# Optimization experiments

Hardware: AMD Instinct MI355X
Metric: run time of the kernel (lower is better)

The kernel has to match this reference:

```python
import jax, jax.numpy as jnp
import numpy as np
import math

HIDDEN = 1024
NUM_HEADS = 16
HEAD_DIM = HIDDEN // NUM_HEADS


def _rope_tables(seq_len, dim, dtype):
    inv_freq = 1.0 / (10000.0 ** (np.arange(0, dim, 2, dtype=np.float32) / dim))
    t = np.arange(seq_len, dtype=np.float32)
    freqs = np.einsum('i,j->ij', t, inv_freq)          # [S, dim/2]
    emb = np.concatenate([freqs, freqs], axis=-1)      # [S, dim]
    return jnp.asarray(np.cos(emb), dtype), jnp.asarray(np.sin(emb), dtype)


def _rotate_half(x):
    x1, x2 = x[..., : x.shape[-1] // 2], x[..., x.shape[-1] // 2:]
    return jnp.concatenate([-x2, x1], axis=-1)


def setup_inputs() -> dict:
    key = jax.random.key(0)
    k1, k2, k3 = jax.random.split(key, 3)
    B, S = 2, 2048
    x = jax.random.normal(k1, (B, S, HIDDEN), dtype=jnp.float32)
    attention_mask = jnp.ones((B, S), dtype=jnp.int32)
    w_qkv = jax.random.normal(k2, (HIDDEN, 3 * HIDDEN), dtype=jnp.float32) * (1.0 / math.sqrt(HIDDEN))
    w_out = jax.random.normal(k3, (HIDDEN, HIDDEN), dtype=jnp.float32) * (1.0 / math.sqrt(HIDDEN))
    return {"x": x, "attention_mask": attention_mask, "w_qkv": w_qkv, "w_out": w_out}


def reference(x, attention_mask, w_qkv, w_out):
    B, S, H = x.shape
    qkv = x @ w_qkv                                   # [B,S,3H]
    qkv = qkv.reshape(B, S, NUM_HEADS, 3 * HEAD_DIM).transpose(0, 2, 1, 3)  # [B,h,S,3d]
    q, k, v = jnp.split(qkv, 3, axis=-1)              # each [B,h,S,d]
    cos, sin = _rope_tables(S, HEAD_DIM, x.dtype)     # [S,d]
    cos = cos[None, None]
    sin = sin[None, None]
    q = q * cos + _rotate_half(q) * sin
    k = k * cos + _rotate_half(k) * sin
    scale = math.sqrt(HEAD_DIM)
    scores = jnp.einsum('bhqd,bhkd->bhqk', q, k) / scale  # [B,h,S,S]
    mask_value = jnp.finfo(scores.dtype).min
    scores = jnp.where(attention_mask[:, None, None, :] == 0, mask_value, scores)
    attn = jax.nn.softmax(scores, axis=-1)
    context = jnp.einsum('bhqk,bhkd->bhqd', attn, v)  # [B,h,S,d]
    context = context.transpose(0, 2, 1, 3).reshape(B, S, H)
    return context @ w_out
```

## Files before the change

### kernel.cpp

```cpp
#include <hip/hip_runtime.h>
#include <hip/hip_bf16.h>
#include <math.h>
#include <stdint.h>


typedef __bf16 bf16;
typedef __bf16 bf16x8 __attribute__((ext_vector_type(8)));
typedef __bf16 bf16x4 __attribute__((ext_vector_type(4)));
typedef float f32x4 __attribute__((ext_vector_type(4)));

#define AS1 __attribute__((address_space(1)))
#define AS3 __attribute__((address_space(3)))

__device__ __forceinline__ void gload_lds16(const void* g, void* l) {
  __builtin_amdgcn_global_load_lds((const AS1 void*)g, (AS3 void*)l, 16, 0, 0);
}

__device__ __forceinline__ f32x4 mfma16(bf16x8 a, bf16x8 b, f32x4 c) {
  return __builtin_amdgcn_mfma_f32_16x16x32_bf16(a, b, c, 0, 0, 0);
}

#define S_LEN 2048


__global__ void k_split_x(const float* __restrict__ x, bf16* __restrict__ xh,
                          bf16* __restrict__ xl) {
  int i = blockIdx.x * 256 + threadIdx.x;
  float4 v = ((const float4*)x)[i];
  float vv[4] = {v.x, v.y, v.z, v.w};
  bf16x4 h, l;
#pragma unroll
  for (int j = 0; j < 4; j++) {
    bf16 hb = (bf16)vv[j];
    h[j] = hb;
    l[j] = (bf16)(vv[j] - (float)hb);
  }
  ((bf16x4*)xh)[i] = h;
  ((bf16x4*)xl)[i] = l;
}

__global__ void k_wt_qkv(const float* __restrict__ w, bf16* __restrict__ bth,
                         bf16* __restrict__ btl) {
  __shared__ float t[32][33];
  int n0 = blockIdx.x * 32, k0 = blockIdx.y * 32;
  int tx = threadIdx.x & 31, ty = threadIdx.x >> 5;
#pragma unroll
  for (int i = 0; i < 4; i++)
    t[ty + 8 * i][tx] = w[(size_t)(k0 + ty + 8 * i) * 3072 + n0 + tx];
  __syncthreads();
#pragma unroll
  for (int i = 0; i < 4; i++) {
    int r = ty + 8 * i;
    float v = t[tx][r];
    size_t o = (size_t)(n0 + r) * 1024 + k0 + tx;
    bf16 hb = (bf16)v;
    bth[o] = hb;
    btl[o] = (bf16)(v - (float)hb);
  }
}

__global__ void k_wt_out(const float* __restrict__ w, bf16* __restrict__ bt) {
  __shared__ float t[32][33];
  int n0 = blockIdx.x * 32, k0 = blockIdx.y * 32;
  int tx = threadIdx.x & 31, ty = threadIdx.x >> 5;
#pragma unroll
  for (int i = 0; i < 4; i++)
    t[ty + 8 * i][tx] = w[(size_t)(k0 + ty + 8 * i) * 1024 + n0 + tx];
  __syncthreads();
#pragma unroll
  for (int i = 0; i < 4; i++) {
    int r = ty + 8 * i;
    bt[(size_t)(n0 + r) * 1024 + k0 + tx] = (bf16)t[tx][r];
  }
}

__global__ void k_rope_tables(float* __restrict__ ct, float* __restrict__ st) {
  int i = blockIdx.x * 256 + threadIdx.x;
  int s = i >> 5, j = i & 31;
  double invf = pow(10000.0, -(double)j / 32.0);
  double a = (double)s * invf;
  ct[i] = (float)cos(a);
  st[i] = (float)sin(a);
}

__global__ __launch_bounds__(256, 2) void k_gemm_qkv(
    const bf16* __restrict__ Ah, const bf16* __restrict__ Al,
    const bf16* __restrict__ Bh, const bf16* __restrict__ Bl,
    bf16* __restrict__ C) {
  const int K = 1024, N = 3072;
  __shared__ __align__(16) bf16 sAh[128 * 32];
  __shared__ __align__(16) bf16 sAl[128 * 32];
  __shared__ __align__(16) bf16 sBh[128 * 32];
  __shared__ __align__(16) bf16 sBl[128 * 32];
  int tid = threadIdx.x, lane = tid & 63, wid = tid >> 6;
  int m0 = blockIdx.x * 128, n0 = blockIdx.y * 128;
  int wm = wid >> 1, wn = wid & 1;

  f32x4 acc[4][4];
#pragma unroll
  for (int a = 0; a < 4; a++)
#pragma unroll
    for (int b = 0; b < 4; b++) acc[a][b] = (f32x4){0.f, 0.f, 0.f, 0.f};

  for (int k0 = 0; k0 < K; k0 += 32) {
#pragma unroll
    for (int p = 0; p < 2; p++) {
      int slot = p * 256 + tid;
      int row = slot >> 2, c16 = slot & 3;
      int cs = c16 ^ ((row >> 1) & 3);
      char* lb = (char*)nullptr;
      int ldsoff = (p * 256 + wid * 64) * 16;
      size_t ga = (size_t)(m0 + row) * K + k0 + cs * 8;
      size_t gb = (size_t)(n0 + row) * K + k0 + cs * 8;
      (void)lb;
      gload_lds16(Ah + ga, (char*)sAh + ldsoff);
      gload_lds16(Al + ga, (char*)sAl + ldsoff);
      gload_lds16(Bh + gb, (char*)sBh + ldsoff);
      gload_lds16(Bl + gb, (char*)sBl + ldsoff);
    }
    __syncthreads();

    bf16x8 fah[4], fal[4], fbh[4], fbl[4];
#pragma unroll
    for (int mf = 0; mf < 4; mf++) {
      int row = wm * 64 + mf * 16 + (lane & 15);
      int c16 = (lane >> 4) ^ ((row >> 1) & 3);
      int off = row * 64 + c16 * 16;
      fah[mf] = *(const bf16x8*)((const char*)sAh + off);
      fal[mf] = *(const bf16x8*)((const char*)sAl + off);
    }
#pragma unroll
    for (int nf = 0; nf < 4; nf++) {
      int row = wn * 64 + nf * 16 + (lane & 15);
      int c16 = (lane >> 4) ^ ((row >> 1) & 3);
      int off = row * 64 + c16 * 16;
      fbh[nf] = *(const bf16x8*)((const char*)sBh + off);
      fbl[nf] = *(const bf16x8*)((const char*)sBl + off);
    }
#pragma unroll
    for (int mf = 0; mf < 4; mf++)
#pragma unroll
      for (int nf = 0; nf < 4; nf++) {
        acc[mf][nf] = mfma16(fah[mf], fbh[nf], acc[mf][nf]);
        acc[mf][nf] = mfma16(fah[mf], fbl[nf], acc[mf][nf]);
        acc[mf][nf] = mfma16(fal[mf], fbh[nf], acc[mf][nf]);
      }
    __syncthreads();
  }

#pragma unroll
  for (int mf = 0; mf < 4; mf++)
#pragma unroll
    for (int nf = 0; nf < 4; nf++)
#pragma unroll
      for (int r = 0; r < 4; r++) {
        int row = m0 + wm * 64 + mf * 16 + (lane >> 4) * 4 + r;
        int col = n0 + wn * 64 + nf * 16 + (lane & 15);
        C[(size_t)row * N + col] = (bf16)acc[mf][nf][r];
      }
}

__global__ void k_rope_scatter(const bf16* __restrict__ QKV,
                               const float* __restrict__ ct,
                               const float* __restrict__ st,
                               bf16* __restrict__ Q, bf16* __restrict__ Kb,
                               bf16* __restrict__ Vt) {
  __shared__ __align__(16) bf16 vt[64 * 64];
  int sblk = blockIdx.x, bh = blockIdx.y;
  int b = bh >> 4, h = bh & 15;
  int tid = threadIdx.x;
  int r = tid >> 2, c = tid & 3;
  int s = sblk * 64 + r;
  size_t rowbase = ((size_t)(b * S_LEN + s)) * 3072 + h * 192;

  bf16x8 qlo = *(const bf16x8*)(QKV + rowbase + c * 8);
  bf16x8 qhi = *(const bf16x8*)(QKV + rowbase + c * 8 + 32);
  bf16x8 klo = *(const bf16x8*)(QKV + rowbase + 64 + c * 8);
  bf16x8 khi = *(const bf16x8*)(QKV + rowbase + 64 + c * 8 + 32);
  bf16x8 vlo = *(const bf16x8*)(QKV + rowbase + 128 + c * 8);
  bf16x8 vhi = *(const bf16x8*)(QKV + rowbase + 128 + c * 8 + 32);

  bf16x8 qol, qoh, kol, koh;
#pragma unroll
  for (int j = 0; j < 8; j++) {
    float cs = ct[s * 32 + c * 8 + j], sn = st[s * 32 + c * 8 + j];
    float q1 = (float)qlo[j], q2 = (float)qhi[j];
    qol[j] = (bf16)(q1 * cs - q2 * sn);
    qoh[j] = (bf16)(q2 * cs + q1 * sn);
    float k1 = (float)klo[j], k2 = (float)khi[j];
    kol[j] = (bf16)(k1 * cs - k2 * sn);
    koh[j] = (bf16)(k2 * cs + k1 * sn);
  }
  size_t qb = ((size_t)bh * S_LEN + s) * 64 + c * 8;
  *(bf16x8*)(Q + qb) = qol;
  *(bf16x8*)(Q + qb + 32) = qoh;
  *(bf16x8*)(Kb + qb) = kol;
  *(bf16x8*)(Kb + qb + 32) = koh;

#pragma unroll
  for (int j = 0; j < 8; j++) {
    vt[(c * 8 + j) * 64 + r] = vlo[j];
    vt[(c * 8 + 32 + j) * 64 + r] = vhi[j];
  }
  __syncthreads();
  int d = tid >> 2, cc = tid & 3;
  size_t vb = ((size_t)bh * 64 + d) * S_LEN + sblk * 64 + cc * 16;
  *(bf16x8*)(Vt + vb) = *(const bf16x8*)(vt + d * 64 + cc * 16);
  *(bf16x8*)(Vt + vb + 8) = *(const bf16x8*)(vt + d * 64 + cc * 16 + 8);
}

__global__ __launch_bounds__(256, 2) void k_attn(
    const bf16* __restrict__ Q, const bf16* __restrict__ Kb,
    const bf16* __restrict__ Vt, const int* __restrict__ mask,
    bf16* __restrict__ Ctx) {
  __shared__ __align__(16) bf16 sK[128 * 64];
  __shared__ __align__(16) bf16 sV[64 * 128];
  __shared__ __align__(16) bf16 sP[4 * 32 * 128];
  int tid = threadIdx.x, lane = tid & 63, wid = tid >> 6;
  int qt = blockIdx.x, bh = blockIdx.y;
  int b = bh >> 4, h = bh & 15;
  int q0 = qt * 128;

  bf16x8 aQ[2][2];
#pragma unroll
  for (int mf = 0; mf < 2; mf++)
#pragma unroll
    for (int ks = 0; ks < 2; ks++) {
      const bf16* p = Q + ((size_t)bh * S_LEN + q0 + wid * 32 + mf * 16 + (lane & 15)) * 64 +
                      ks * 32 + (lane >> 4) * 8;
      bf16x8 v = *(const bf16x8*)p;
#pragma unroll
      for (int j = 0; j < 8; j++) v[j] = (bf16)((float)v[j] * 0.125f);
      aQ[mf][ks] = v;
    }

  f32x4 O[2][4];
  float mrow[2][4], lrow[2][4];
#pragma unroll
  for (int mf = 0; mf < 2; mf++)
#pragma unroll
    for (int nd = 0; nd < 4; nd++) O[mf][nd] = (f32x4){0.f, 0.f, 0.f, 0.f};
#pragma unroll
  for (int mf = 0; mf < 2; mf++)
#pragma unroll
    for (int r = 0; r < 4; r++) { mrow[mf][r] = -3e38f; lrow[mf][r] = 0.f; }

  for (int kt = 0; kt < 16; kt++) {
    int k0 = kt * 128;
#pragma unroll
    for (int p = 0; p < 4; p++) {
      int slot = p * 256 + tid;
      int row = slot >> 3, c16 = slot & 7;
      int cs = c16 ^ (row & 7);
      gload_lds16(Kb + ((size_t)bh * S_LEN + k0 + row) * 64 + cs * 8,
                  (char*)sK + (p * 256 + wid * 64) * 16);
    }
#pragma unroll
    for (int p = 0; p < 4; p++) {
      int slot = p * 256 + tid;
      int row = slot >> 4, c16 = slot & 15;
      int cs = c16 ^ (row & 7);
      gload_lds16(Vt + ((size_t)bh * 64 + row) * S_LEN + k0 + cs * 8,
                  (char*)sV + (p * 256 + wid * 64) * 16);
    }
    __syncthreads();

    f32x4 sfr[2][8];
#pragma unroll
    for (int mf = 0; mf < 2; mf++)
#pragma unroll
      for (int nf = 0; nf < 8; nf++) sfr[mf][nf] = (f32x4){0.f, 0.f, 0.f, 0.f};
#pragma unroll
    for (int nf = 0; nf < 8; nf++) {
#pragma unroll
      for (int ks = 0; ks < 2; ks++) {
        int row = nf * 16 + (lane & 15);
        int c16 = (ks * 4 + (lane >> 4)) ^ (row & 7);
        bf16x8 bk = *(const bf16x8*)((const char*)sK + row * 128 + c16 * 16);
        sfr[0][nf] = mfma16(aQ[0][ks], bk, sfr[0][nf]);
        sfr[1][nf] = mfma16(aQ[1][ks], bk, sfr[1][nf]);
      }
    }
#pragma unroll
    for (int nf = 0; nf < 8; nf++) {
      int kpos = k0 + nf * 16 + (lane & 15);
      if (mask[b * S_LEN + kpos] == 0) {
#pragma unroll
        for (int r = 0; r < 4; r++) { sfr[0][nf][r] = -1e30f; sfr[1][nf][r] = -1e30f; }
      }
    }
    float alpha[2][4];
#pragma unroll
    for (int mf = 0; mf < 2; mf++)
#pragma unroll
      for (int r = 0; r < 4; r++) {
        float mx = -3e38f;
#pragma unroll
        for (int nf = 0; nf < 8; nf++) mx = fmaxf(mx, sfr[mf][nf][r]);
#pragma unroll
        for (int off = 1; off < 16; off <<= 1) mx = fmaxf(mx, __shfl_xor(mx, off, 64));
        float mnew = fmaxf(mrow[mf][r], mx);
        float a = __expf(mrow[mf][r] - mnew);
        mrow[mf][r] = mnew;
        float psum = 0.f;
#pragma unroll
        for (int nf = 0; nf < 8; nf++) {
          float p0 = __expf(sfr[mf][nf][r] - mnew);
          sfr[mf][nf][r] = p0;
          psum += p0;
        }
#pragma unroll
        for (int off = 1; off < 16; off <<= 1) psum += __shfl_xor(psum, off, 64);
        lrow[mf][r] = lrow[mf][r] * a + psum;
        alpha[mf][r] = a;
      }
#pragma unroll
    for (int mf = 0; mf < 2; mf++)
#pragma unroll
      for (int nd = 0; nd < 4; nd++)
#pragma unroll
        for (int r = 0; r < 4; r++) O[mf][nd][r] *= alpha[mf][r];

    char* pw = (char*)sP + wid * 32 * 256;
#pragma unroll
    for (int mf = 0; mf < 2; mf++)
#pragma unroll
      for (int r = 0; r < 4; r++) {
        int row = mf * 16 + (lane >> 4) * 4 + r;
#pragma unroll
        for (int nf = 0; nf < 8; nf++) {
          int col = nf * 16 + (lane & 15);
          int c16 = (col >> 3) ^ (row & 7);
          *(bf16*)(pw + row * 256 + c16 * 16 + (col & 7) * 2) = (bf16)sfr[mf][nf][r];
        }
      }
#pragma unroll
    for (int ks = 0; ks < 4; ks++) {
      bf16x8 aP[2];
#pragma unroll
      for (int mf = 0; mf < 2; mf++) {
        int row = mf * 16 + (lane & 15);
        int c16 = (ks * 4 + (lane >> 4)) ^ (row & 7);
        aP[mf] = *(const bf16x8*)(pw + row * 256 + c16 * 16);
      }
#pragma unroll
      for (int nd = 0; nd < 4; nd++) {
        int row = nd * 16 + (lane & 15);
        int c16 = (ks * 4 + (lane >> 4)) ^ (row & 7);
        bf16x8 bv = *(const bf16x8*)((const char*)sV + row * 256 + c16 * 16);
#pragma unroll
        for (int mf = 0; mf < 2; mf++) O[mf][nd] = mfma16(aP[mf], bv, O[mf][nd]);
      }
    }
    __syncthreads();
  }

#pragma unroll
  for (int mf = 0; mf < 2; mf++)
#pragma unroll
    for (int r = 0; r < 4; r++) {
      float inv = 1.f / lrow[mf][r];
      int srow = q0 + wid * 32 + mf * 16 + (lane >> 4) * 4 + r;
#pragma unroll
      for (int nd = 0; nd < 4; nd++) {
        int d = nd * 16 + (lane & 15);
        Ctx[((size_t)b * S_LEN + srow) * 1024 + h * 64 + d] = (bf16)(O[mf][nd][r] * inv);
      }
    }
}

__global__ __launch_bounds__(256, 2) void k_gemm_out(
    const bf16* __restrict__ A, const bf16* __restrict__ Bt,
    float* __restrict__ C) {
  const int K = 1024, N = 1024;
  __shared__ __align__(16) bf16 sA[128 * 32];
  __shared__ __align__(16) bf16 sB[128 * 32];
  int tid = threadIdx.x, lane = tid & 63, wid = tid >> 6;
  int m0 = blockIdx.x * 128, n0 = blockIdx.y * 128;
  int wm = wid >> 1, wn = wid & 1;

  f32x4 acc[4][4];
#pragma unroll
  for (int a = 0; a < 4; a++)
#pragma unroll
    for (int b = 0; b < 4; b++) acc[a][b] = (f32x4){0.f, 0.f, 0.f, 0.f};

  for (int k0 = 0; k0 < K; k0 += 32) {
#pragma unroll
    for (int p = 0; p < 2; p++) {
      int slot = p * 256 + tid;
      int row = slot >> 2, c16 = slot & 3;
      int cs = c16 ^ ((row >> 1) & 3);
      int ldsoff = (p * 256 + wid * 64) * 16;
      gload_lds16(A + (size_t)(m0 + row) * K + k0 + cs * 8, (char*)sA + ldsoff);
      gload_lds16(Bt + (size_t)(n0 + row) * K + k0 + cs * 8, (char*)sB + ldsoff);
    }
    __syncthreads();
    bf16x8 fa[4], fb[4];
#pragma unroll
    for (int mf = 0; mf < 4; mf++) {
      int row = wm * 64 + mf * 16 + (lane & 15);
      int c16 = (lane >> 4) ^ ((row >> 1) & 3);
      fa[mf] = *(const bf16x8*)((const char*)sA + row * 64 + c16 * 16);
    }
#pragma unroll
    for (int nf = 0; nf < 4; nf++) {
      int row = wn * 64 + nf * 16 + (lane & 15);
      int c16 = (lane >> 4) ^ ((row >> 1) & 3);
      fb[nf] = *(const bf16x8*)((const char*)sB + row * 64 + c16 * 16);
    }
#pragma unroll
    for (int mf = 0; mf < 4; mf++)
#pragma unroll
      for (int nf = 0; nf < 4; nf++)
        acc[mf][nf] = mfma16(fa[mf], fb[nf], acc[mf][nf]);
    __syncthreads();
  }
#pragma unroll
  for (int mf = 0; mf < 4; mf++)
#pragma unroll
    for (int nf = 0; nf < 4; nf++)
#pragma unroll
      for (int r = 0; r < 4; r++) {
        int row = m0 + wm * 64 + mf * 16 + (lane >> 4) * 4 + r;
        int col = n0 + wn * 64 + nf * 16 + (lane & 15);
        C[(size_t)row * N + col] = acc[mf][nf][r];
      }
}

extern "C" void kernel_launch(void* const* d_in, const int* in_sizes, int n_in,
                              void* d_out, int out_size, void* d_ws, size_t ws_size,
                              hipStream_t stream) {
  const float* x = (const float*)d_in[0];
  const int* mask = (const int*)d_in[1];
  const float* wqkv = (const float*)d_in[2];
  const float* wout = (const float*)d_in[3];
  float* out = (float*)d_out;
  char* ws = (char*)d_ws;

  bf16* Xh  = (bf16*)(ws + 0);
  bf16* Xl  = (bf16*)(ws + 8388608);
  bf16* Wqh = (bf16*)(ws + 16777216);
  bf16* Wql = (bf16*)(ws + 23068672);
  bf16* Wo  = (bf16*)(ws + 29360128);
  bf16* QKV = (bf16*)(ws + 31457280);
  bf16* Qb  = (bf16*)(ws + 56623104);
  bf16* Kb  = (bf16*)(ws + 65011712);
  bf16* Vt  = (bf16*)(ws + 73400320);
  bf16* Ctx = (bf16*)(ws + 81788928);
  float* ct = (float*)(ws + 90177536);
  float* st = (float*)(ws + 90439680);

  k_split_x<<<4096, 256, 0, stream>>>(x, Xh, Xl);
  k_wt_qkv<<<dim3(96, 32), 256, 0, stream>>>(wqkv, Wqh, Wql);
  k_wt_out<<<dim3(32, 32), 256, 0, stream>>>(wout, Wo);
  k_rope_tables<<<256, 256, 0, stream>>>(ct, st);
  k_gemm_qkv<<<dim3(32, 24), 256, 0, stream>>>(Xh, Xl, Wqh, Wql, QKV);
  k_rope_scatter<<<dim3(32, 32), 256, 0, stream>>>(QKV, ct, st, Qb, Kb, Vt);
  k_attn<<<dim3(16, 32), 256, 0, stream>>>(Qb, Kb, Vt, mask, Ctx);
  k_gemm_out<<<dim3(32, 8), 256, 0, stream>>>(Ctx, Wo, out);
}
```

Measured before the change: 285.9 us.

## Transpose attention MFMAs to keep P in registers and drop LDS staging

The attention kernel now computes S^T = K·Q^T, so each lane holds scores for a single query row across keys. Softmax reductions need only two cross-lane shuffles instead of four per row, and the probability tile feeds the PV MFMA straight from registers, which removes the sP shared-memory buffer and its scattered bf16 writes. Mask loads become int4 vectors, output stores become bf16x4, and launch bounds ask for 3 blocks per CU now that less LDS is used. In exchange V is read from LDS as two bf16x4 halves per fragment, and the tighter launch bound may force register spills.

```diff
diff --git a/kernel.cpp b/kernel.cpp
--- a/kernel.cpp
+++ b/kernel.cpp
@@ -108,11 +108,9 @@
       int slot = p * 256 + tid;
       int row = slot >> 2, c16 = slot & 3;
       int cs = c16 ^ ((row >> 1) & 3);
-      char* lb = (char*)nullptr;
       int ldsoff = (p * 256 + wid * 64) * 16;
       size_t ga = (size_t)(m0 + row) * K + k0 + cs * 8;
       size_t gb = (size_t)(n0 + row) * K + k0 + cs * 8;
-      (void)lb;
       gload_lds16(Ah + ga, (char*)sAh + ldsoff);
       gload_lds16(Al + ga, (char*)sAl + ldsoff);
       gload_lds16(Bh + gb, (char*)sBh + ldsoff);
@@ -209,41 +207,39 @@
   *(bf16x8*)(Vt + vb + 8) = *(const bf16x8*)(vt + d * 64 + cc * 16 + 8);
 }
 
-__global__ __launch_bounds__(256, 2) void k_attn(
+__global__ __launch_bounds__(256, 3) void k_attn(
     const bf16* __restrict__ Q, const bf16* __restrict__ Kb,
     const bf16* __restrict__ Vt, const int* __restrict__ mask,
     bf16* __restrict__ Ctx) {
   __shared__ __align__(16) bf16 sK[128 * 64];
   __shared__ __align__(16) bf16 sV[64 * 128];
-  __shared__ __align__(16) bf16 sP[4 * 32 * 128];
   int tid = threadIdx.x, lane = tid & 63, wid = tid >> 6;
+  int g = lane >> 4, q = lane & 15;
   int qt = blockIdx.x, bh = blockIdx.y;
   int b = bh >> 4, h = bh & 15;
-  int q0 = qt * 128;
-
-  bf16x8 aQ[2][2];
+  int q0 = qt * 128 + wid * 32;
+
+  bf16x8 bQ[2][2];
 #pragma unroll
   for (int mf = 0; mf < 2; mf++)
 #pragma unroll
     for (int ks = 0; ks < 2; ks++) {
-      const bf16* p = Q + ((size_t)bh * S_LEN + q0 + wid * 32 + mf * 16 + (lane & 15)) * 64 +
-                      ks * 32 + (lane >> 4) * 8;
+      const bf16* p = Q + ((size_t)bh * S_LEN + q0 + mf * 16 + q) * 64 + ks * 32 + g * 8;
       bf16x8 v = *(const bf16x8*)p;
 #pragma unroll
       for (int j = 0; j < 8; j++) v[j] = (bf16)((float)v[j] * 0.125f);
-      aQ[mf][ks] = v;
+      bQ[mf][ks] = v;
     }
 
   f32x4 O[2][4];
-  float mrow[2][4], lrow[2][4];
-#pragma unroll
-  for (int mf = 0; mf < 2; mf++)
+  float mrow[2], lrow[2];
+#pragma unroll
+  for (int mf = 0; mf < 2; mf++) {
 #pragma unroll
     for (int nd = 0; nd < 4; nd++) O[mf][nd] = (f32x4){0.f, 0.f, 0.f, 0.f};
-#pragma unroll
-  for (int mf = 0; mf < 2; mf++)
-#pragma unroll
-    for (int r = 0; r < 4; r++) { mrow[mf][r] = -3e38f; lrow[mf][r] = 0.f; }
+    mrow[mf] = -3e38f;
+    lrow[mf] = 0.f;
+  }
 
   for (int kt = 0; kt < 16; kt++) {
     int k0 = kt * 128;
@@ -269,104 +265,96 @@
 #pragma unroll
     for (int mf = 0; mf < 2; mf++)
 #pragma unroll
-      for (int nf = 0; nf < 8; nf++) sfr[mf][nf] = (f32x4){0.f, 0.f, 0.f, 0.f};
-#pragma unroll
-    for (int nf = 0; nf < 8; nf++) {
+      for (int kf = 0; kf < 8; kf++) sfr[mf][kf] = (f32x4){0.f, 0.f, 0.f, 0.f};
+#pragma unroll
+    for (int kf = 0; kf < 8; kf++) {
 #pragma unroll
       for (int ks = 0; ks < 2; ks++) {
-        int row = nf * 16 + (lane & 15);
-        int c16 = (ks * 4 + (lane >> 4)) ^ (row & 7);
-        bf16x8 bk = *(const bf16x8*)((const char*)sK + row * 128 + c16 * 16);
-        sfr[0][nf] = mfma16(aQ[0][ks], bk, sfr[0][nf]);
-        sfr[1][nf] = mfma16(aQ[1][ks], bk, sfr[1][nf]);
+        int row = kf * 16 + q;
+        int c16 = (ks * 4 + g) ^ (row & 7);
+        bf16x8 ak = *(const bf16x8*)((const char*)sK + row * 128 + c16 * 16);
+        sfr[0][kf] = mfma16(ak, bQ[0][ks], sfr[0][kf]);
+        sfr[1][kf] = mfma16(ak, bQ[1][ks], sfr[1][kf]);
       }
     }
 #pragma unroll
-    for (int nf = 0; nf < 8; nf++) {
-      int kpos = k0 + nf * 16 + (lane & 15);
-      if (mask[b * S_LEN + kpos] == 0) {
-#pragma unroll
-        for (int r = 0; r < 4; r++) { sfr[0][nf][r] = -1e30f; sfr[1][nf][r] = -1e30f; }
+    for (int kf = 0; kf < 8; kf++) {
+      int4 mv = *(const int4*)(mask + b * S_LEN + k0 + kf * 16 + g * 4);
+      int mm[4] = {mv.x, mv.y, mv.z, mv.w};
+#pragma unroll
+      for (int r = 0; r < 4; r++)
+        if (mm[r] == 0) { sfr[0][kf][r] = -1e30f; sfr[1][kf][r] = -1e30f; }
+    }
+    float alpha[2];
+#pragma unroll
+    for (int mf = 0; mf < 2; mf++) {
+      float mx = -3e38f;
+#pragma unroll
+      for (int kf = 0; kf < 8; kf++)
+#pragma unroll
+        for (int r = 0; r < 4; r++) mx = fmaxf(mx, sfr[mf][kf][r]);
+      mx = fmaxf(mx, __shfl_xor(mx, 16, 64));
+      mx = fmaxf(mx, __shfl_xor(mx, 32, 64));
+      float mnew = fmaxf(mrow[mf], mx);
+      float al = __expf(mrow[mf] - mnew);
+      mrow[mf] = mnew;
+      float ps = 0.f;
+#pragma unroll
+      for (int kf = 0; kf < 8; kf++)
+#pragma unroll
+        for (int r = 0; r < 4; r++) {
+          float p0 = __expf(sfr[mf][kf][r] - mnew);
+          sfr[mf][kf][r] = p0;
+          ps += p0;
+        }
+      ps += __shfl_xor(ps, 16, 64);
+      ps += __shfl_xor(ps, 32, 64);
+      lrow[mf] = lrow[mf] * al + ps;
+      alpha[mf] = al;
+    }
+#pragma unroll
+    for (int mf = 0; mf < 2; mf++)
+#pragma unroll
+      for (int nd = 0; nd < 4; nd++)
+#pragma unroll
+        for (int r = 0; r < 4; r++) O[mf][nd][r] *= alpha[mf];
+
+#pragma unroll
+    for (int ks = 0; ks < 4; ks++) {
+      bf16x8 pb[2];
+#pragma unroll
+      for (int mf = 0; mf < 2; mf++)
+#pragma unroll
+        for (int j = 0; j < 8; j++)
+          pb[mf][j] = (bf16)sfr[mf][2 * ks + (j >> 2)][j & 3];
+#pragma unroll
+      for (int nd = 0; nd < 4; nd++) {
+        int row = nd * 16 + q;
+        int sw = (row & 7) << 4;
+        bf16x4 v0 = *(const bf16x4*)((const char*)sV + row * 256 + ((ks * 64 + g * 8) ^ sw));
+        bf16x4 v1 = *(const bf16x4*)((const char*)sV + row * 256 + ((ks * 64 + g * 8 + 32) ^ sw));
+        bf16x8 av;
+#pragma unroll
+        for (int j = 0; j < 4; j++) { av[j] = v0[j]; av[4 + j] = v1[j]; }
+#pragma unroll
+        for (int mf = 0; mf < 2; mf++) O[mf][nd] = mfma16(av, pb[mf], O[mf][nd]);
       }
     }
-    float alpha[2][4];
-#pragma unroll
-    for (int mf = 0; mf < 2; mf++)
-#pragma unroll
-      for (int r = 0; r < 4; r++) {
-        float mx = -3e38f;
-#pragma unroll
-        for (int nf = 0; nf < 8; nf++) mx = fmaxf(mx, sfr[mf][nf][r]);
-#pragma unroll
-        for (int off = 1; off < 16; off <<= 1) mx = fmaxf(mx, __shfl_xor(mx, off, 64));
-        float mnew = fmaxf(mrow[mf][r], mx);
-        float a = __expf(mrow[mf][r] - mnew);
-        mrow[mf][r] = mnew;
-        float psum = 0.f;
-#pragma unroll
-        for (int nf = 0; nf < 8; nf++) {
-          float p0 = __expf(sfr[mf][nf][r] - mnew);
-          sfr[mf][nf][r] = p0;
-          psum += p0;
-        }
-#pragma unroll
-        for (int off = 1; off < 16; off <<= 1) psum += __shfl_xor(psum, off, 64);
-        lrow[mf][r] = lrow[mf][r] * a + psum;
-        alpha[mf][r] = a;
-      }
-#pragma unroll
-    for (int mf = 0; mf < 2; mf++)
-#pragma unroll
-      for (int nd = 0; nd < 4; nd++)
-#pragma unroll
-        for (int r = 0; r < 4; r++) O[mf][nd][r] *= alpha[mf][r];
-
-    char* pw = (char*)sP + wid * 32 * 256;
-#pragma unroll
-    for (int mf = 0; mf < 2; mf++)
-#pragma unroll
-      for (int r = 0; r < 4; r++) {
-        int row = mf * 16 + (lane >> 4) * 4 + r;
-#pragma unroll
-        for (int nf = 0; nf < 8; nf++) {
-          int col = nf * 16 + (lane & 15);
-          int c16 = (col >> 3) ^ (row & 7);
-          *(bf16*)(pw + row * 256 + c16 * 16 + (col & 7) * 2) = (bf16)sfr[mf][nf][r];
-        }
-      }
-#pragma unroll
-    for (int ks = 0; ks < 4; ks++) {
-      bf16x8 aP[2];
-#pragma unroll
-      for (int mf = 0; mf < 2; mf++) {
-        int row = mf * 16 + (lane & 15);
-        int c16 = (ks * 4 + (lane >> 4)) ^ (row & 7);
-        aP[mf] = *(const bf16x8*)(pw + row * 256 + c16 * 16);
-      }
-#pragma unroll
-      for (int nd = 0; nd < 4; nd++) {
-        int row = nd * 16 + (lane & 15);
-        int c16 = (ks * 4 + (lane >> 4)) ^ (row & 7);
-        bf16x8 bv = *(const bf16x8*)((const char*)sV + row * 256 + c16 * 16);
-#pragma unroll
-        for (int mf = 0; mf < 2; mf++) O[mf][nd] = mfma16(aP[mf], bv, O[mf][nd]);
-      }
-    }
-    __syncthreads();
-  }
-
-#pragma unroll
-  for (int mf = 0; mf < 2; mf++)
-#pragma unroll
-    for (int r = 0; r < 4; r++) {
-      float inv = 1.f / lrow[mf][r];
-      int srow = q0 + wid * 32 + mf * 16 + (lane >> 4) * 4 + r;
-#pragma unroll
-      for (int nd = 0; nd < 4; nd++) {
-        int d = nd * 16 + (lane & 15);
-        Ctx[((size_t)b * S_LEN + srow) * 1024 + h * 64 + d] = (bf16)(O[mf][nd][r] * inv);
-      }
-    }
+    __syncthreads();
+  }
+
+#pragma unroll
+  for (int mf = 0; mf < 2; mf++) {
+    float inv = 1.f / lrow[mf];
+    int srow = q0 + mf * 16 + q;
+#pragma unroll
+    for (int nd = 0; nd < 4; nd++) {
+      bf16x4 o4;
+#pragma unroll
+      for (int r = 0; r < 4; r++) o4[r] = (bf16)(O[mf][nd][r] * inv);
+      *(bf16x4*)(Ctx + ((size_t)b * S_LEN + srow) * 1024 + h * 64 + nd * 16 + g * 4) = o4;
+    }
+  }
 }
 
 __global__ __launch_bounds__(256, 2) void k_gemm_out(
```

Result: faster. 265.3 us (-7.2%).
